# Optimization experiments

Hardware: AMD Instinct MI355X
Metric: run time of the kernel (lower is better)

## Reference

```python
import jax, jax.numpy as jnp
import numpy as np

B, C, H, W = 8, 128, 64, 64
K = 3
MID = C // 4  # reduction=4


def setup_inputs() -> dict:
    key = jax.random.key(0)
    ks = jax.random.split(key, 8)
    f = lambda k, s, sc=1.0: jax.random.normal(k, s, dtype=jnp.float32) * sc
    return {
        "X2": f(ks[0], (B, C, H, W)),
        "Y2": f(ks[1], (B, C, H, W)),
        "static_w": f(ks[2], (C, 1, K, K), 0.1),        # depthwise conv weight (OIHW, groups=C)
        "w1": f(ks[3], (2 * MID, 2 * C), 0.05),          # context_conv1 1x1
        "w2": f(ks[4], (2 * MID, 2 * MID), 0.05),        # context_conv2 1x1
        "w3": f(ks[5], (C * K * K, 2 * MID), 0.05),      # context_conv3 1x1
        "ws": f(ks[6], (K * K, 2 * C), 0.05),            # spatial_conv 1x1
        "wf": f(ks[7], (C, 2 * C), 0.05),                # fusion_conv 1x1
    }


def _c1x1(w, x):
    # 1x1 conv, no bias: (O,I) x (B,I,H,W) -> (B,O,H,W)
    return jnp.einsum('oc,bchw->bohw', w, x)


def reference(X2, Y2, static_w, w1, w2, w3, ws, wf):
    Bn, Cn, Hn, Wn = X2.shape
    Kn = static_w.shape[-1]
    pad = (Kn - 1) // 2

    # static depthwise conv
    Xs = jax.lax.conv_general_dilated(
        X2, static_w, window_strides=(1, 1), padding='SAME',
        feature_group_count=Cn, dimension_numbers=('NCHW', 'OIHW', 'NCHW'))

    Fc = jnp.concatenate([Xs, Y2], axis=1)  # (B, 2C, H, W)

    # SE-style context branch: 1x1 conv -> global avg pool -> 1x1 -> relu -> 1x1
    ctx = _c1x1(w1, Fc).mean(axis=(2, 3))                  # (B, 2*mid)
    ctx = jax.nn.relu(jnp.einsum('oc,bc->bo', w2, ctx))    # (B, 2*mid)
    channel_filter = jnp.einsum('oc,bc->bo', w3, ctx)      # (B, C*k*k)
    channel_filter = channel_filter.reshape(Bn, Cn, Kn * Kn, 1, 1)

    spatial_filter = _c1x1(ws, Fc).reshape(Bn, 1, Kn * Kn, Hn, Wn)
    dynamic_filter = channel_filter + spatial_filter       # (B, C, k*k, H, W)

    # unfold X2: patch order matches F.unfold (channel-major, kernel row-major)
    Xp = jnp.pad(X2, ((0, 0), (0, 0), (pad, pad), (pad, pad)))
    patches = jnp.stack(
        [Xp[:, :, i:i + Hn, j:j + Wn] for i in range(Kn) for j in range(Kn)],
        axis=2)                                            # (B, C, k*k, H, W)

    dynamic_out = (patches * dynamic_filter).sum(axis=2)   # (B, C, H, W)

    out = _c1x1(wf, jnp.concatenate([Xs, dynamic_out], axis=1))
    return out
```

## Files before the change

kernel.cpp:

```cpp
#include <hip/hip_runtime.h>
#include <hip/hip_bf16.h>

#define Bn 8
#define Cn 128
#define Hn 64
#define Wn 64
#define HWn 4096
#define KK 9

typedef short short8 __attribute__((ext_vector_type(8)));
typedef float f32x4 __attribute__((ext_vector_type(4)));

__device__ inline unsigned short f2b(float v) {
    __hip_bfloat16 h = __float2bfloat16(v);
    return *reinterpret_cast<unsigned short*>(&h);
}

__global__ __launch_bounds__(256) void k_pre(
    const float* __restrict__ X2, const float* __restrict__ Y2,
    float* __restrict__ pws)
{
    int bc = blockIdx.x, t = threadIdx.x;
    const float4* xp = (const float4*)(X2 + (size_t)bc * HWn);
    const float4* yp = (const float4*)(Y2 + (size_t)bc * HWn);
    float v[6] = {0.f, 0.f, 0.f, 0.f, 0.f, 0.f};
#pragma unroll
    for (int i = 0; i < 4; i++) {
        int q = t + i * 256;
        float4 x = xp[q], y = yp[q];
        float s4 = x.x + x.y + x.z + x.w;
        v[0] += s4;
        v[5] += y.x + y.y + y.z + y.w;
        int px = q * 4, h = px >> 6, w4 = px & 63;
        if (h == 0)   v[1] += s4;
        if (h == 63)  v[2] += s4;
        if (w4 == 0)  v[3] += x.x;
        if (w4 == 60) v[4] += x.w;
    }
#pragma unroll
    for (int k = 0; k < 6; k++)
#pragma unroll
        for (int off = 32; off; off >>= 1)
            v[k] += __shfl_down(v[k], off);
    __shared__ float red[4][6];
    int lane = t & 63, wv = t >> 6;
    if (lane == 0) {
#pragma unroll
        for (int k = 0; k < 6; k++) red[wv][k] = v[k];
    }
    __syncthreads();
    if (t < 6) pws[bc * 6 + t] = red[0][t] + red[1][t] + red[2][t] + red[3][t];
}

__global__ __launch_bounds__(256) void k_ctx(
    const float* __restrict__ X2, const float* __restrict__ pws,
    const float* __restrict__ sw,
    const float* __restrict__ w1, const float* __restrict__ w2,
    const float* __restrict__ w3, const float* __restrict__ wf,
    const float* __restrict__ wsp, float* __restrict__ cf,
    unsigned short* __restrict__ wfb, unsigned short* __restrict__ wsb)
{
    int b = blockIdx.x, t = threadIdx.x;
    {
        int boff = b * 4096;
        for (int i = t; i < 4096; i += 256) wfb[boff + i] = f2b(wf[boff + i]);
        for (int i = t; i < 512; i += 256) {
            int j = b * 512 + i, tt = j >> 8, c = j & 255;
            wsb[j] = (tt < KK) ? f2b(wsp[tt * 256 + c]) : (unsigned short)0;
        }
    }
    __shared__ float mfc[256], c1[64], c2[64];
    if (t < 128) {
        int bc = b * Cn + t;
        const float* S = pws + bc * 6;
        const float* pl = X2 + (size_t)bc * HWn;
        float T = S[0];
        float R[3]  = { S[2], 0.f, S[1] };
        float Cc[3] = { S[4], 0.f, S[3] };
        float x00 = pl[0], x063 = pl[63], x630 = pl[63 * 64], x6363 = pl[4095];
        float Xc[3][3] = {{x6363, 0.f, x630}, {0.f, 0.f, 0.f}, {x063, 0.f, x00}};
        float a = 0.f;
#pragma unroll
        for (int i = 0; i < 3; i++)
#pragma unroll
            for (int j = 0; j < 3; j++)
                a += sw[t * 9 + i * 3 + j] * (T - R[i] - Cc[j] + Xc[i][j]);
        mfc[t] = a * (1.f / HWn);
    } else {
        mfc[t] = pws[(b * Cn + (t - 128)) * 6 + 5] * (1.f / HWn);
    }
    __syncthreads();
    if (t < 64) {
        const float4* wr = (const float4*)(w1 + t * 256);
        float a = 0.f;
        for (int c = 0; c < 64; c++) {
            float4 v = wr[c];
            a += v.x * mfc[c*4] + v.y * mfc[c*4+1] + v.z * mfc[c*4+2] + v.w * mfc[c*4+3];
        }
        c1[t] = a;
    }
    __syncthreads();
    if (t < 64) {
        const float4* wr = (const float4*)(w2 + t * 64);
        float a = 0.f;
        for (int c = 0; c < 16; c++) {
            float4 v = wr[c];
            a += v.x * c1[c*4] + v.y * c1[c*4+1] + v.z * c1[c*4+2] + v.w * c1[c*4+3];
        }
        c2[t] = fmaxf(a, 0.f);
    }
    __syncthreads();
    for (int j = t; j < Cn * KK; j += 256) {
        const float4* wr = (const float4*)(w3 + j * 64);
        float a = 0.f;
        for (int c = 0; c < 16; c++) {
            float4 v = wr[c];
            a += v.x * c2[c*4] + v.y * c2[c*4+1] + v.z * c2[c*4+2] + v.w * c2[c*4+3];
        }
        cf[b * Cn * KK + j] = a;
    }
}

__global__ __launch_bounds__(256, 4) void k_main(
    const float* __restrict__ X2, const float* __restrict__ Y2,
    const float* __restrict__ sw,
    const unsigned short* __restrict__ wfb, const unsigned short* __restrict__ wsb,
    const float* __restrict__ cf, float* __restrict__ out)
{
    __shared__ unsigned short sFt[2][32][Cn];
    __shared__ float sSf[KK][32];
    __shared__ float sCf[Cn * KK];
    __shared__ float sSw[Cn * KK];

    int bid = blockIdx.x;
    int b = bid & 7, rest = bid >> 3;
    int wh = rest & 1, h = rest >> 1;
    int w0 = wh * 32;
    int t = threadIdx.x;
    int w = t & 31, cg = t >> 5;
    int wg = w0 + w;
    int swz = (w & 7) << 3;

    for (int i = t; i < Cn * KK; i += 256) {
        sSw[i] = sw[i];
        sCf[i] = cf[b * Cn * KK + i];
    }
    __syncthreads();

    const float* xbase = X2 + (size_t)b * Cn * HWn + h * Wn + wg;
    const float* ybase = Y2 + (size_t)b * Cn * HWn + h * Wn + wg;
    bool hm = h > 0, hp = h < Hn - 1;
    bool wm = wg > 0, wp = wg < Wn - 1;

    {
        unsigned int px0 = 0, px1 = 0, py0 = 0, py1 = 0;
#pragma unroll 4
        for (int i = 0; i < 16; i++) {
            int c = cg * 16 + i;
            const float* xp = xbase + (size_t)c * HWn;
            float tp[9];
            tp[0] = (hm && wm) ? xp[-Wn - 1] : 0.f;
            tp[1] = hm ? xp[-Wn] : 0.f;
            tp[2] = (hm && wp) ? xp[-Wn + 1] : 0.f;
            tp[3] = wm ? xp[-1] : 0.f;
            tp[4] = xp[0];
            tp[5] = wp ? xp[1] : 0.f;
            tp[6] = (hp && wm) ? xp[Wn - 1] : 0.f;
            tp[7] = hp ? xp[Wn] : 0.f;
            tp[8] = (hp && wp) ? xp[Wn + 1] : 0.f;
            const float* wkp = sSw + c * 9;
            float a = 0.f;
#pragma unroll
            for (int q = 0; q < 9; q++) a += tp[q] * wkp[q];
            float yv = ybase[(size_t)c * HWn];
            unsigned int ah = f2b(a), yh = f2b(yv);
            int sub = i & 3;
            if (sub == 0)      { px0 = ah;        py0 = yh; }
            else if (sub == 1) { px0 |= ah << 16; py0 |= yh << 16; }
            else if (sub == 2) { px1 = ah;        py1 = yh; }
            else {
                px1 |= ah << 16;  py1 |= yh << 16;
                int col = (c - 3) ^ swz;
                uint2 qx; qx.x = px0; qx.y = px1;
                uint2 qy; qy.x = py0; qy.y = py1;
                *(uint2*)(&sFt[0][w][col]) = qx;
                *(uint2*)(&sFt[1][w][col]) = qy;
            }
        }
    }
    __syncthreads();

    {
        int lane = t & 63, wv = t >> 6;
        int l16 = lane & 15, half = lane >> 4, kk = half * 8;
        if (wv < 2) {
            int wA = wv * 16 + l16;
            int swzA = (wA & 7) << 3;
            f32x4 acc = (f32x4){0.f, 0.f, 0.f, 0.f};
#pragma unroll
            for (int ks = 0; ks < 8; ks++) {
                short8 av = *(const short8*)(wsb + l16 * 256 + ks * 32 + kk);
                int col = (((ks & 3) * 32 + kk)) ^ swzA;
                short8 bv = *(const short8*)(&sFt[ks >> 2][wA][0] + col);
                acc = __builtin_amdgcn_mfma_f32_16x16x32_bf16(av, bv, acc, 0, 0, 0);
            }
#pragma unroll
            for (int r = 0; r < 4; r++) {
                int tt = half * 4 + r;
                if (tt < KK) sSf[tt][wA] = acc[r];
            }
        }
    }
    __syncthreads();

    {
        float sfw[9];
#pragma unroll
        for (int q = 0; q < 9; q++) sfw[q] = sSf[q][w];
        unsigned int p0 = 0, p1 = 0;
#pragma unroll 4
        for (int i = 0; i < 16; i++) {
            int c = cg * 16 + i;
            const float* xp = xbase + (size_t)c * HWn;
            float tp[9];
            tp[0] = (hm && wm) ? xp[-Wn - 1] : 0.f;
            tp[1] = hm ? xp[-Wn] : 0.f;
            tp[2] = (hm && wp) ? xp[-Wn + 1] : 0.f;
            tp[3] = wm ? xp[-1] : 0.f;
            tp[4] = xp[0];
            tp[5] = wp ? xp[1] : 0.f;
            tp[6] = (hp && wm) ? xp[Wn - 1] : 0.f;
            tp[7] = hp ? xp[Wn] : 0.f;
            tp[8] = (hp && wp) ? xp[Wn + 1] : 0.f;
            const float* cfp = sCf + c * 9;
            float a = 0.f;
#pragma unroll
            for (int q = 0; q < 9; q++) a += tp[q] * (cfp[q] + sfw[q]);
            unsigned int ah = f2b(a);
            int sub = i & 3;
            if (sub == 0)      p0 = ah;
            else if (sub == 1) p0 |= ah << 16;
            else if (sub == 2) p1 = ah;
            else {
                p1 |= ah << 16;
                int col = (c - 3) ^ swz;
                uint2 q2; q2.x = p0; q2.y = p1;
                *(uint2*)(&sFt[1][w][col]) = q2;
            }
        }
    }
    __syncthreads();

    {
        int lane = t & 63, wv = t >> 6;
        int l16 = lane & 15, half = lane >> 4, kk = half * 8;
        f32x4 acc[2][2];
#pragma unroll
        for (int m = 0; m < 2; m++)
#pragma unroll
            for (int n = 0; n < 2; n++)
                acc[m][n] = (f32x4){0.f, 0.f, 0.f, 0.f};
#pragma unroll
        for (int ks = 0; ks < 8; ks++) {
            int bufi = ks >> 2;
            int kc = (ks & 3) * 32 + kk;
            short8 bfrag[2];
#pragma unroll
            for (int n = 0; n < 2; n++) {
                int wB = n * 16 + l16;
                int col = kc ^ ((wB & 7) << 3);
                bfrag[n] = *(const short8*)(&sFt[bufi][wB][0] + col);
            }
#pragma unroll
            for (int m = 0; m < 2; m++) {
                short8 av = *(const short8*)(
                    wfb + ((wv * 32 + m * 16 + l16) * 256 + ks * 32 + kk));
#pragma unroll
                for (int n = 0; n < 2; n++)
                    acc[m][n] = __builtin_amdgcn_mfma_f32_16x16x32_bf16(
                        av, bfrag[n], acc[m][n], 0, 0, 0);
            }
        }
        size_t obase = (size_t)b * Cn * HWn + (size_t)h * Wn + w0;
#pragma unroll
        for (int m = 0; m < 2; m++)
#pragma unroll
            for (int n = 0; n < 2; n++)
#pragma unroll
                for (int r = 0; r < 4; r++) {
                    int o = wv * 32 + m * 16 + half * 4 + r;
                    out[obase + (size_t)o * HWn + n * 16 + l16] = acc[m][n][r];
                }
    }
}

extern "C" void kernel_launch(void* const* d_in, const int* in_sizes, int n_in,
                              void* d_out, int out_size, void* d_ws, size_t ws_size,
                              hipStream_t stream) {
    (void)in_sizes; (void)n_in; (void)out_size; (void)ws_size;
    const float* X2  = (const float*)d_in[0];
    const float* Y2  = (const float*)d_in[1];
    const float* sw  = (const float*)d_in[2];
    const float* w1  = (const float*)d_in[3];
    const float* w2  = (const float*)d_in[4];
    const float* w3  = (const float*)d_in[5];
    const float* wsp = (const float*)d_in[6];
    const float* wf  = (const float*)d_in[7];
    float* out = (float*)d_out;

    float* wsf = (float*)d_ws;
    float* pws = wsf;
    float* cf  = wsf + 6144;
    unsigned short* wfb = (unsigned short*)(wsf + 15360);
    unsigned short* wsb = (unsigned short*)(wsf + 31744);

    hipLaunchKernelGGL(k_pre, dim3(Bn * Cn), dim3(256), 0, stream, X2, Y2, pws);
    hipLaunchKernelGGL(k_ctx, dim3(Bn), dim3(256), 0, stream,
                       X2, pws, sw, w1, w2, w3, wf, wsp, cf, wfb, wsb);
    hipLaunchKernelGGL(k_main, dim3(Bn * Hn * 2), dim3(256), 0, stream,
                       X2, Y2, sw, wfb, wsb, cf, out);
}
```

Before: 56.53 us.

## Widen main tile to full rows, share taps via shuffles, split ctx kernel

The main kernel now has each 512-thread block cover a full 64-wide row instead of half a row. Each thread loads only three vertical taps per channel and gets the horizontal neighbours through lane shuffles. Those taps stay in registers and are reused by the dynamic-filter pass instead of being reloaded from global memory. k_pre also gathers the four corner pixels so k_ctx no longer reads X2, and k_ctx is spread over 32 blocks instead of 8. The intent is to cut redundant global loads and raise context-kernel parallelism, at the cost of higher register pressure (48 floats of taps) and larger blocks that may lower occupancy.

```diff
diff --git a/kernel.cpp b/kernel.cpp
--- a/kernel.cpp
+++ b/kernel.cpp
@@ -23,7 +23,9 @@
     int bc = blockIdx.x, t = threadIdx.x;
     const float4* xp = (const float4*)(X2 + (size_t)bc * HWn);
     const float4* yp = (const float4*)(Y2 + (size_t)bc * HWn);
-    float v[6] = {0.f, 0.f, 0.f, 0.f, 0.f, 0.f};
+    float v[10];
+#pragma unroll
+    for (int k = 0; k < 10; k++) v[k] = 0.f;
 #pragma unroll
     for (int i = 0; i < 4; i++) {
         int q = t + i * 256;
@@ -36,49 +38,53 @@
         if (h == 63)  v[2] += s4;
         if (w4 == 0)  v[3] += x.x;
         if (w4 == 60) v[4] += x.w;
-    }
-#pragma unroll
-    for (int k = 0; k < 6; k++)
+        if (px == 0)    v[6] += x.x;
+        if (px == 60)   v[7] += x.w;
+        if (px == 4032) v[8] += x.x;
+        if (px == 4092) v[9] += x.w;
+    }
+#pragma unroll
+    for (int k = 0; k < 10; k++)
 #pragma unroll
         for (int off = 32; off; off >>= 1)
             v[k] += __shfl_down(v[k], off);
-    __shared__ float red[4][6];
+    __shared__ float red[4][10];
     int lane = t & 63, wv = t >> 6;
     if (lane == 0) {
 #pragma unroll
-        for (int k = 0; k < 6; k++) red[wv][k] = v[k];
-    }
-    __syncthreads();
-    if (t < 6) pws[bc * 6 + t] = red[0][t] + red[1][t] + red[2][t] + red[3][t];
+        for (int k = 0; k < 10; k++) red[wv][k] = v[k];
+    }
+    __syncthreads();
+    if (t < 10) pws[bc * 10 + t] = red[0][t] + red[1][t] + red[2][t] + red[3][t];
 }
 
 __global__ __launch_bounds__(256) void k_ctx(
-    const float* __restrict__ X2, const float* __restrict__ pws,
-    const float* __restrict__ sw,
+    const float* __restrict__ pws, const float* __restrict__ sw,
     const float* __restrict__ w1, const float* __restrict__ w2,
     const float* __restrict__ w3, const float* __restrict__ wf,
     const float* __restrict__ wsp, float* __restrict__ cf,
     unsigned short* __restrict__ wfb, unsigned short* __restrict__ wsb)
 {
-    int b = blockIdx.x, t = threadIdx.x;
-    {
-        int boff = b * 4096;
-        for (int i = t; i < 4096; i += 256) wfb[boff + i] = f2b(wf[boff + i]);
-        for (int i = t; i < 512; i += 256) {
-            int j = b * 512 + i, tt = j >> 8, c = j & 255;
+    int blk = blockIdx.x, b = blk >> 2, qd = blk & 3;
+    int t = threadIdx.x;
+    for (int i = t; i < 1024; i += 256) {
+        int j = blk * 1024 + i;
+        wfb[j] = f2b(wf[j]);
+    }
+    {
+        int j = blk * 128 + t;
+        if (t < 128) {
+            int tt = j >> 8, c = j & 255;
             wsb[j] = (tt < KK) ? f2b(wsp[tt * 256 + c]) : (unsigned short)0;
         }
     }
     __shared__ float mfc[256], c1[64], c2[64];
     if (t < 128) {
-        int bc = b * Cn + t;
-        const float* S = pws + bc * 6;
-        const float* pl = X2 + (size_t)bc * HWn;
+        const float* S = pws + (b * Cn + t) * 10;
         float T = S[0];
         float R[3]  = { S[2], 0.f, S[1] };
         float Cc[3] = { S[4], 0.f, S[3] };
-        float x00 = pl[0], x063 = pl[63], x630 = pl[63 * 64], x6363 = pl[4095];
-        float Xc[3][3] = {{x6363, 0.f, x630}, {0.f, 0.f, 0.f}, {x063, 0.f, x00}};
+        float Xc[3][3] = {{S[9], 0.f, S[8]}, {0.f, 0.f, 0.f}, {S[7], 0.f, S[6]}};
         float a = 0.f;
 #pragma unroll
         for (int i = 0; i < 3; i++)
@@ -87,7 +93,7 @@
                 a += sw[t * 9 + i * 3 + j] * (T - R[i] - Cc[j] + Xc[i][j]);
         mfc[t] = a * (1.f / HWn);
     } else {
-        mfc[t] = pws[(b * Cn + (t - 128)) * 6 + 5] * (1.f / HWn);
+        mfc[t] = pws[(b * Cn + (t - 128)) * 10 + 5] * (1.f / HWn);
     }
     __syncthreads();
     if (t < 64) {
@@ -110,7 +116,7 @@
         c2[t] = fmaxf(a, 0.f);
     }
     __syncthreads();
-    for (int j = t; j < Cn * KK; j += 256) {
+    for (int j = qd * 288 + t; j < qd * 288 + 288; j += 256) {
         const float4* wr = (const float4*)(w3 + j * 64);
         float a = 0.f;
         for (int c = 0; c < 16; c++) {
@@ -121,70 +127,68 @@
     }
 }
 
-__global__ __launch_bounds__(256, 4) void k_main(
+__global__ __launch_bounds__(512, 4) void k_main(
     const float* __restrict__ X2, const float* __restrict__ Y2,
     const float* __restrict__ sw,
     const unsigned short* __restrict__ wfb, const unsigned short* __restrict__ wsb,
     const float* __restrict__ cf, float* __restrict__ out)
 {
-    __shared__ unsigned short sFt[2][32][Cn];
-    __shared__ float sSf[KK][32];
-    __shared__ float sCf[Cn * KK];
-    __shared__ float sSw[Cn * KK];
+    __shared__ unsigned short sFt[2][Wn][Cn];
+    __shared__ float sSf[KK][Wn];
+    __shared__ float sCfP[Cn][12];
+    __shared__ float sSwP[Cn][12];
 
     int bid = blockIdx.x;
-    int b = bid & 7, rest = bid >> 3;
-    int wh = rest & 1, h = rest >> 1;
-    int w0 = wh * 32;
+    int b = bid & 7, h = bid >> 3;
     int t = threadIdx.x;
-    int w = t & 31, cg = t >> 5;
-    int wg = w0 + w;
+    int w = t & 63, cg = t >> 6;
     int swz = (w & 7) << 3;
-
-    for (int i = t; i < Cn * KK; i += 256) {
-        sSw[i] = sw[i];
-        sCf[i] = cf[b * Cn * KK + i];
-    }
-    __syncthreads();
-
-    const float* xbase = X2 + (size_t)b * Cn * HWn + h * Wn + wg;
-    const float* ybase = Y2 + (size_t)b * Cn * HWn + h * Wn + wg;
+    int c0 = cg * 16;
+
+    for (int i = t; i < Cn * KK; i += 512) {
+        int c = i / 9, q = i - c * 9;
+        sSwP[c][q] = sw[i];
+        sCfP[c][q] = cf[b * Cn * KK + i];
+    }
+    __syncthreads();
+
+    const float* xcol = X2 + (size_t)(b * Cn + c0) * HWn + h * Wn + w;
+    const float* ycol = Y2 + (size_t)(b * Cn + c0) * HWn + h * Wn + w;
     bool hm = h > 0, hp = h < Hn - 1;
-    bool wm = wg > 0, wp = wg < Wn - 1;
-
-    {
-        unsigned int px0 = 0, px1 = 0, py0 = 0, py1 = 0;
-#pragma unroll 4
+    bool wm = w > 0, wp = w < Wn - 1;
+
+    float tap[16][3];
+
+    {
+        unsigned int px[4], py[4];
+#pragma unroll
         for (int i = 0; i < 16; i++) {
-            int c = cg * 16 + i;
-            const float* xp = xbase + (size_t)c * HWn;
-            float tp[9];
-            tp[0] = (hm && wm) ? xp[-Wn - 1] : 0.f;
-            tp[1] = hm ? xp[-Wn] : 0.f;
-            tp[2] = (hm && wp) ? xp[-Wn + 1] : 0.f;
-            tp[3] = wm ? xp[-1] : 0.f;
-            tp[4] = xp[0];
-            tp[5] = wp ? xp[1] : 0.f;
-            tp[6] = (hp && wm) ? xp[Wn - 1] : 0.f;
-            tp[7] = hp ? xp[Wn] : 0.f;
-            tp[8] = (hp && wp) ? xp[Wn + 1] : 0.f;
-            const float* wkp = sSw + c * 9;
-            float a = 0.f;
-#pragma unroll
-            for (int q = 0; q < 9; q++) a += tp[q] * wkp[q];
-            float yv = ybase[(size_t)c * HWn];
+            int c = c0 + i;
+            const float* xp = xcol + (size_t)i * HWn;
+            float r0 = hm ? xp[-Wn] : 0.f;
+            float r1 = xp[0];
+            float r2 = hp ? xp[Wn] : 0.f;
+            tap[i][0] = r0; tap[i][1] = r1; tap[i][2] = r2;
+            float4 k0 = *(const float4*)&sSwP[c][0];
+            float4 k1 = *(const float4*)&sSwP[c][4];
+            float  k8 = sSwP[c][8];
+            float xl0 = __shfl_up(r0, 1), xr0 = __shfl_down(r0, 1);
+            float xl1 = __shfl_up(r1, 1), xr1 = __shfl_down(r1, 1);
+            float xl2 = __shfl_up(r2, 1), xr2 = __shfl_down(r2, 1);
+            if (!wm) { xl0 = 0.f; xl1 = 0.f; xl2 = 0.f; }
+            if (!wp) { xr0 = 0.f; xr1 = 0.f; xr2 = 0.f; }
+            float a = k0.x * xl0 + k0.y * r0 + k0.z * xr0
+                    + k0.w * xl1 + k1.x * r1 + k1.y * xr1
+                    + k1.z * xl2 + k1.w * r2 + k8 * xr2;
+            float yv = ycol[(size_t)i * HWn];
             unsigned int ah = f2b(a), yh = f2b(yv);
-            int sub = i & 3;
-            if (sub == 0)      { px0 = ah;        py0 = yh; }
-            else if (sub == 1) { px0 |= ah << 16; py0 |= yh << 16; }
-            else if (sub == 2) { px1 = ah;        py1 = yh; }
-            else {
-                px1 |= ah << 16;  py1 |= yh << 16;
-                int col = (c - 3) ^ swz;
-                uint2 qx; qx.x = px0; qx.y = px1;
-                uint2 qy; qy.x = py0; qy.y = py1;
-                *(uint2*)(&sFt[0][w][col]) = qx;
-                *(uint2*)(&sFt[1][w][col]) = qy;
+            int sub = i & 7;
+            if ((sub & 1) == 0) { px[sub >> 1] = ah; py[sub >> 1] = yh; }
+            else { px[sub >> 1] |= ah << 16; py[sub >> 1] |= yh << 16; }
+            if (sub == 7) {
+                int col = (c - 7) ^ swz;
+                *(uint4*)(&sFt[0][w][col]) = *(uint4*)px;
+                *(uint4*)(&sFt[1][w][col]) = *(uint4*)py;
             }
         }
     }
@@ -193,7 +197,7 @@
     {
         int lane = t & 63, wv = t >> 6;
         int l16 = lane & 15, half = lane >> 4, kk = half * 8;
-        if (wv < 2) {
+        if (wv < 4) {
             int wA = wv * 16 + l16;
             int swzA = (wA & 7) << 3;
             f32x4 acc = (f32x4){0.f, 0.f, 0.f, 0.f};
@@ -217,35 +221,29 @@
         float sfw[9];
 #pragma unroll
         for (int q = 0; q < 9; q++) sfw[q] = sSf[q][w];
-        unsigned int p0 = 0, p1 = 0;
-#pragma unroll 4
+        unsigned int pd[4];
+#pragma unroll
         for (int i = 0; i < 16; i++) {
-            int c = cg * 16 + i;
-            const float* xp = xbase + (size_t)c * HWn;
-            float tp[9];
-            tp[0] = (hm && wm) ? xp[-Wn - 1] : 0.f;
-            tp[1] = hm ? xp[-Wn] : 0.f;
-            tp[2] = (hm && wp) ? xp[-Wn + 1] : 0.f;
-            tp[3] = wm ? xp[-1] : 0.f;
-            tp[4] = xp[0];
-            tp[5] = wp ? xp[1] : 0.f;
-            tp[6] = (hp && wm) ? xp[Wn - 1] : 0.f;
-            tp[7] = hp ? xp[Wn] : 0.f;
-            tp[8] = (hp && wp) ? xp[Wn + 1] : 0.f;
-            const float* cfp = sCf + c * 9;
-            float a = 0.f;
-#pragma unroll
-            for (int q = 0; q < 9; q++) a += tp[q] * (cfp[q] + sfw[q]);
+            int c = c0 + i;
+            float r0 = tap[i][0], r1 = tap[i][1], r2 = tap[i][2];
+            float4 e0 = *(const float4*)&sCfP[c][0];
+            float4 e1 = *(const float4*)&sCfP[c][4];
+            float  e8 = sCfP[c][8];
+            float xl0 = __shfl_up(r0, 1), xr0 = __shfl_down(r0, 1);
+            float xl1 = __shfl_up(r1, 1), xr1 = __shfl_down(r1, 1);
+            float xl2 = __shfl_up(r2, 1), xr2 = __shfl_down(r2, 1);
+            if (!wm) { xl0 = 0.f; xl1 = 0.f; xl2 = 0.f; }
+            if (!wp) { xr0 = 0.f; xr1 = 0.f; xr2 = 0.f; }
+            float a = (e0.x + sfw[0]) * xl0 + (e0.y + sfw[1]) * r0 + (e0.z + sfw[2]) * xr0
+                    + (e0.w + sfw[3]) * xl1 + (e1.x + sfw[4]) * r1 + (e1.y + sfw[5]) * xr1
+                    + (e1.z + sfw[6]) * xl2 + (e1.w + sfw[7]) * r2 + (e8 + sfw[8]) * xr2;
             unsigned int ah = f2b(a);
-            int sub = i & 3;
-            if (sub == 0)      p0 = ah;
-            else if (sub == 1) p0 |= ah << 16;
-            else if (sub == 2) p1 = ah;
-            else {
-                p1 |= ah << 16;
-                int col = (c - 3) ^ swz;
-                uint2 q2; q2.x = p0; q2.y = p1;
-                *(uint2*)(&sFt[1][w][col]) = q2;
+            int sub = i & 7;
+            if ((sub & 1) == 0) pd[sub >> 1] = ah;
+            else pd[sub >> 1] |= ah << 16;
+            if (sub == 7) {
+                int col = (c - 7) ^ swz;
+                *(uint4*)(&sFt[1][w][col]) = *(uint4*)pd;
             }
         }
     }
@@ -254,43 +252,31 @@
     {
         int lane = t & 63, wv = t >> 6;
         int l16 = lane & 15, half = lane >> 4, kk = half * 8;
-        f32x4 acc[2][2];
-#pragma unroll
-        for (int m = 0; m < 2; m++)
-#pragma unroll
-            for (int n = 0; n < 2; n++)
-                acc[m][n] = (f32x4){0.f, 0.f, 0.f, 0.f};
+        int o0 = wv * 16;
+        f32x4 acc[4];
+#pragma unroll
+        for (int n = 0; n < 4; n++) acc[n] = (f32x4){0.f, 0.f, 0.f, 0.f};
 #pragma unroll
         for (int ks = 0; ks < 8; ks++) {
             int bufi = ks >> 2;
             int kc = (ks & 3) * 32 + kk;
-            short8 bfrag[2];
-#pragma unroll
-            for (int n = 0; n < 2; n++) {
+            short8 av = *(const short8*)(wfb + (o0 + l16) * 256 + ks * 32 + kk);
+#pragma unroll
+            for (int n = 0; n < 4; n++) {
                 int wB = n * 16 + l16;
                 int col = kc ^ ((wB & 7) << 3);
-                bfrag[n] = *(const short8*)(&sFt[bufi][wB][0] + col);
-            }
-#pragma unroll
-            for (int m = 0; m < 2; m++) {
-                short8 av = *(const short8*)(
-                    wfb + ((wv * 32 + m * 16 + l16) * 256 + ks * 32 + kk));
-#pragma unroll
-                for (int n = 0; n < 2; n++)
-                    acc[m][n] = __builtin_amdgcn_mfma_f32_16x16x32_bf16(
-                        av, bfrag[n], acc[m][n], 0, 0, 0);
-            }
-        }
-        size_t obase = (size_t)b * Cn * HWn + (size_t)h * Wn + w0;
-#pragma unroll
-        for (int m = 0; m < 2; m++)
-#pragma unroll
-            for (int n = 0; n < 2; n++)
-#pragma unroll
-                for (int r = 0; r < 4; r++) {
-                    int o = wv * 32 + m * 16 + half * 4 + r;
-                    out[obase + (size_t)o * HWn + n * 16 + l16] = acc[m][n][r];
-                }
+                short8 bv = *(const short8*)(&sFt[bufi][wB][0] + col);
+                acc[n] = __builtin_amdgcn_mfma_f32_16x16x32_bf16(av, bv, acc[n], 0, 0, 0);
+            }
+        }
+        size_t obase = (size_t)b * Cn * HWn + (size_t)h * Wn;
+#pragma unroll
+        for (int n = 0; n < 4; n++)
+#pragma unroll
+            for (int r = 0; r < 4; r++) {
+                int o = o0 + half * 4 + r;
+                out[obase + (size_t)o * HWn + n * 16 + l16] = acc[n][r];
+            }
     }
 }
 
@@ -310,13 +296,13 @@
 
     float* wsf = (float*)d_ws;
     float* pws = wsf;
-    float* cf  = wsf + 6144;
-    unsigned short* wfb = (unsigned short*)(wsf + 15360);
-    unsigned short* wsb = (unsigned short*)(wsf + 31744);
+    float* cf  = wsf + 10240;
+    unsigned short* wfb = (unsigned short*)(wsf + 19456);
+    unsigned short* wsb = (unsigned short*)(wsf + 35840);
 
     hipLaunchKernelGGL(k_pre, dim3(Bn * Cn), dim3(256), 0, stream, X2, Y2, pws);
-    hipLaunchKernelGGL(k_ctx, dim3(Bn), dim3(256), 0, stream,
-                       X2, pws, sw, w1, w2, w3, wf, wsp, cf, wfb, wsb);
-    hipLaunchKernelGGL(k_main, dim3(Bn * Hn * 2), dim3(256), 0, stream,
+    hipLaunchKernelGGL(k_ctx, dim3(32), dim3(256), 0, stream,
+                       pws, sw, w1, w2, w3, wf, wsp, cf, wfb, wsb);
+    hipLaunchKernelGGL(k_main, dim3(Bn * Hn), dim3(512), 0, stream,
                        X2, Y2, sw, wfb, wsb, cf, out);
 }
```

Measured after the change: 60.77 us. 7.5% more time.
